# Optimization experiments

Hardware: AMD Instinct MI355X
Metric: run time of the kernel (lower is better)

## Reference

```python
import jax, jax.numpy as jnp
import numpy as np

EPS = 1e-7
FEAT_DIM = 128
N_DATA = 100000
NCE_K = 16384
NCE_T = 0.07


def _l2norm(x):
    # Normalize(power=2): x / (sum(x^2, axis=1)^(1/2))
    return x / jnp.sqrt(jnp.sum(x * x, axis=1, keepdims=True))


def _embed(x, W, b):
    return _l2norm(x @ W.T + b)


def _contrast_loss(x, n_data):
    # x: [B, K+1] of (unnormalized) probabilities; col 0 = positive
    bsz = x.shape[0]
    m = x.shape[1] - 1
    Pn = 1.0 / float(n_data)
    c = m * Pn + EPS
    log_D1 = jnp.log(x[:, 0] / (x[:, 0] + c))          # positives
    log_D0 = jnp.log((m * Pn) / (x[:, 1:] + c))         # negatives
    return -(log_D1.sum() + log_D0.sum()) / bsz


def setup_inputs() -> dict:
    key = jax.random.key(0)
    ks = jax.random.split(key, 10)
    s_dim, t_dim = 1024, 2048
    B = 64
    stdv = 1.0 / np.sqrt(FEAT_DIM / 3.0)
    inp = {
        "f_s": jax.random.normal(ks[0], (B, s_dim), dtype=jnp.float32),
        "f_t": jax.random.normal(ks[1], (B, t_dim), dtype=jnp.float32),
        "idx": jax.random.randint(ks[2], (B,), 0, N_DATA),
        "contrast_idx": jax.random.randint(ks[3], (B, NCE_K + 1), 0, N_DATA),
        # Embed params (linear): Linear(dim_in, feat_dim)
        "Ws": jax.random.normal(ks[4], (FEAT_DIM, s_dim), dtype=jnp.float32) / np.sqrt(s_dim),
        "bs": jnp.zeros((FEAT_DIM,), dtype=jnp.float32),
        "Wt": jax.random.normal(ks[5], (FEAT_DIM, t_dim), dtype=jnp.float32) / np.sqrt(t_dim),
        "bt": jnp.zeros((FEAT_DIM,), dtype=jnp.float32),
        # memory banks, init uniform(-stdv, stdv) as in CRD ContrastMemory
        "memory_v1": jax.random.uniform(ks[6], (N_DATA, FEAT_DIM), jnp.float32, -stdv, stdv),
        "memory_v2": jax.random.uniform(ks[7], (N_DATA, FEAT_DIM), jnp.float32, -stdv, stdv),
    }
    return inp


def reference(f_s, f_t, idx, contrast_idx, Ws, bs, Wt, bt, memory_v1, memory_v2):
    v_s = _embed(f_s, Ws, bs)   # [B, D]
    v_t = _embed(f_t, Wt, bt)   # [B, D]

    # idx.select(1,0).copy_(y): column 0 is the positive index
    idx_all = jnp.concatenate([idx[:, None], contrast_idx[:, 1:]], axis=1)  # [B, K+1]

    # gather from memory banks + bmm similarity
    w1 = memory_v1[idx_all]   # [B, K+1, D] (v_t side bank)
    w2 = memory_v2[idx_all]   # [B, K+1, D] (v_s side bank)
    out_t = jnp.exp(jnp.einsum('bkd,bd->bk', w1, v_t) / NCE_T)  # out_v2
    out_s = jnp.exp(jnp.einsum('bkd,bd->bk', w2, v_s) / NCE_T)  # out_v1

    # Z set on first batch: Z = out.mean() * n_data (detached constant)
    Z_s = jax.lax.stop_gradient(out_s.mean()) * N_DATA
    Z_t = jax.lax.stop_gradient(out_t.mean()) * N_DATA
    out_s = out_s / Z_s
    out_t = out_t / Z_t

    s_loss = _contrast_loss(out_s, N_DATA)
    t_loss = _contrast_loss(out_t, N_DATA)
    return s_loss + t_loss
```

## Files before the change

### kernel.cpp

```cpp
#include <hip/hip_runtime.h>

#define NDATA 100000
#define KP1 16385
#define BSZ 64
#define PTOT (BSZ * KP1)
#define NCHUNKS 6250
#define INV_T (1.0f / 0.07f)
#define ACC_STRIDE 64
#define ACC_GROUPS 32
#define SG_NWAVES 1024
#define SG_NITER 7

typedef short short8 __attribute__((ext_vector_type(8)));
typedef float f32x4 __attribute__((ext_vector_type(4)));

__device__ __forceinline__ float wave_reduce64(float v) {
    #pragma unroll
    for (int off = 32; off >= 1; off >>= 1) v += __shfl_xor(v, off);
    return v;
}

__device__ __forceinline__ float group_reduce16(float v) {
    v += __shfl_xor(v, 8); v += __shfl_xor(v, 4);
    v += __shfl_xor(v, 2); v += __shfl_xor(v, 1);
    return v;
}

__device__ __forceinline__ unsigned short f2bf(float f) {
    unsigned u = __float_as_uint(f);
    u += 0x7FFFu + ((u >> 16) & 1u);
    return (unsigned short)(u >> 16);
}

__device__ __forceinline__ float bfm(float x) {
    return __uint_as_float(((unsigned)f2bf(x)) << 16);
}

__device__ __forceinline__ short8 pack_bf16(float4 lo, float4 hi) {
    short8 r;
    r[0] = (short)f2bf(lo.x); r[1] = (short)f2bf(lo.y);
    r[2] = (short)f2bf(lo.z); r[3] = (short)f2bf(lo.w);
    r[4] = (short)f2bf(hi.x); r[5] = (short)f2bf(hi.y);
    r[6] = (short)f2bf(hi.z); r[7] = (short)f2bf(hi.w);
    return r;
}

__device__ __forceinline__ float dot4(float4 a, float4 b, float acc) {
    acc = fmaf(a.x, b.x, acc);
    acc = fmaf(a.y, b.y, acc);
    acc = fmaf(a.z, b.z, acc);
    return fmaf(a.w, b.w, acc);
}

__device__ __forceinline__ float dot8bf(const float4* a, const float4* v, int li, float d) {
    #pragma unroll
    for (int h = 0; h < 2; ++h) {
        const float4 x = a[li * 2 + h], y = v[li * 2 + h];
        d = fmaf(bfm(x.x), bfm(y.x), d);
        d = fmaf(bfm(x.y), bfm(y.y), d);
        d = fmaf(bfm(x.z), bfm(y.z), d);
        d = fmaf(bfm(x.w), bfm(y.w), d);
    }
    return d;
}

__global__ __launch_bounds__(256) void embed_kernel(
    const float* __restrict__ fs, const float* __restrict__ ft,
    const float* __restrict__ Ws, const float* __restrict__ bs,
    const float* __restrict__ Wt, const float* __restrict__ bt,
    float* __restrict__ vraw_s, float* __restrict__ vraw_t)
{
    __shared__ __align__(16) float4 FS[512];
    __shared__ __align__(16) float4 FT[1024];

    const int t  = threadIdx.x;
    const int b0 = blockIdx.y * 2;

    for (int q = t; q < 512; q += 256) {
        const int b = q >> 8, i = q & 255;
        FS[q] = ((const float4*)(fs + (size_t)(b0 + b) * 1024))[i];
    }
    for (int q = t; q < 1024; q += 256) {
        const int b = q >> 9, i = q & 511;
        FT[q] = ((const float4*)(ft + (size_t)(b0 + b) * 2048))[i];
    }
    __syncthreads();

    const int w = t >> 6, lane = t & 63;
    const int d = blockIdx.x * 4 + w;

    {
        const float4* wrow = (const float4*)(Ws + (size_t)d * 1024);
        float a0 = 0.0f, a1 = 0.0f;
        #pragma unroll
        for (int i = 0; i < 4; ++i) {
            const float4 wv = wrow[i * 64 + lane];
            a0 = dot4(wv, FS[i * 64 + lane], a0);
            a1 = dot4(wv, FS[256 + i * 64 + lane], a1);
        }
        a0 = wave_reduce64(a0) + bs[d];
        a1 = wave_reduce64(a1) + bs[d];
        if (lane == 0) {
            vraw_s[(size_t)b0 * 128 + d]       = a0;
            vraw_s[(size_t)(b0 + 1) * 128 + d] = a1;
        }
    }
    {
        const float4* wrow = (const float4*)(Wt + (size_t)d * 2048);
        float a0 = 0.0f, a1 = 0.0f;
        #pragma unroll
        for (int i = 0; i < 8; ++i) {
            const float4 wv = wrow[i * 64 + lane];
            a0 = dot4(wv, FT[i * 64 + lane], a0);
            a1 = dot4(wv, FT[512 + i * 64 + lane], a1);
        }
        a0 = wave_reduce64(a0) + bt[d];
        a1 = wave_reduce64(a1) + bt[d];
        if (lane == 0) {
            vraw_t[(size_t)b0 * 128 + d]       = a0;
            vraw_t[(size_t)(b0 + 1) * 128 + d] = a1;
        }
    }
}

__global__ __launch_bounds__(256) void norm_kernel(
    const float* __restrict__ vraw_t, const float* __restrict__ vraw_s,
    float* __restrict__ sct, float* __restrict__ scs)
{
    const float* __restrict__ v = blockIdx.x ? vraw_s : vraw_t;
    float* __restrict__ sc      = blockIdx.x ? scs : sct;
    const int t = threadIdx.x, b = t >> 2, g = t & 3;
    const float4* row = (const float4*)(v + (size_t)b * 128 + g * 32);
    float s = 0.0f;
    #pragma unroll
    for (int j = 0; j < 8; ++j) s = dot4(row[j], row[j], s);
    s += __shfl_xor(s, 1);
    s += __shfl_xor(s, 2);
    if (g == 0) sc[b] = INV_T * rsqrtf(s);
}

__global__ __launch_bounds__(256) void hist_kernel(
    const int* __restrict__ cidx, unsigned* __restrict__ cnt)
{
    const int b = blockIdx.x, part = blockIdx.y, t = threadIdx.x;
    const unsigned inc = 1u << ((b & 3) * 8);
    const int w = b >> 2;
    const int kbase = part * 1024 + 1;
    #pragma unroll
    for (int j = 0; j < 4; ++j) {
        const int row = cidx[(size_t)b * KP1 + kbase + j * 256 + t];
        atomicAdd(&cnt[(size_t)row * 16 + w], inc);
    }
}

#define SG_ISSUE(AB, CB, VM, CID)                                            \
  {                                                                          \
    const int cc_ = ((CID) < NCHUNKS) ? (CID) : (NCHUNKS - 1);               \
    VM = ((CID) < NCHUNKS) ? ~0u : 0u;                                       \
    const int r0_ = cc_ << 4;                                                \
    const float4* ar_ = (const float4*)(bankp + (size_t)(r0_ + m) * 128);    \
    _Pragma("unroll")                                                        \
    for (int kk = 0; kk < 4; ++kk) {                                         \
      AB[kk * 2]     = ar_[(kk * 4 + q4) * 2];                               \
      AB[kk * 2 + 1] = ar_[(kk * 4 + q4) * 2 + 1];                           \
    }                                                                        \
    _Pragma("unroll")                                                        \
    for (int n = 0; n < 4; ++n)                                              \
      CB[n] = cnt[(size_t)(r0_ + m) * 16 + n * 4 + q4];                      \
  }

#define SG_PROCESS(AB, CB, VM)                                               \
  {                                                                          \
    short8 af_[4];                                                           \
    _Pragma("unroll")                                                        \
    for (int kk = 0; kk < 4; ++kk)                                           \
      af_[kk] = pack_bf16(AB[kk * 2], AB[kk * 2 + 1]);                       \
    _Pragma("unroll")                                                        \
    for (int n = 0; n < 4; ++n) {                                            \
      f32x4 av = {0.f, 0.f, 0.f, 0.f};                                       \
      _Pragma("unroll")                                                      \
      for (int kk = 0; kk < 4; ++kk)                                         \
        av = __builtin_amdgcn_mfma_f32_16x16x32_bf16(bfv[n][kk], af_[kk], av, 0, 0, 0); \
      const unsigned cw_ = CB[n] & VM;                                       \
      _Pragma("unroll")                                                      \
      for (int j = 0; j < 4; ++j) {                                          \
        const float fm_ = (float)((cw_ >> (8 * j)) & 255u);                  \
        const float e_  = __expf(av[j] * scv[n][j]);                         \
        se  = fmaf(e_, fm_, se);                                             \
        se2 = fmaf(e_ * fm_, e_, se2);                                       \
      }                                                                      \
    }                                                                        \
  }

__global__ __launch_bounds__(256) void sgemm_kernel(
    const float* __restrict__ m1, const float* __restrict__ m2,
    const float* __restrict__ vraw_s, const float* __restrict__ vraw_t,
    const float* __restrict__ sct, const float* __restrict__ scs,
    const unsigned* __restrict__ cnt,
    float* __restrict__ acc)
{
    const int t = threadIdx.x;
    const int bank = blockIdx.y;
    const float* __restrict__ bankp = bank ? m2 : m1;
    const float* __restrict__ vp    = bank ? vraw_s : vraw_t;
    const float* __restrict__ scp   = bank ? scs : sct;

    const int lane = t & 63;
    const int m  = lane & 15;
    const int q4 = lane >> 4;

    short8 bfv[4][4];
    #pragma unroll
    for (int n = 0; n < 4; ++n) {
        const float4* vrow = (const float4*)(vp + (size_t)(n * 16 + m) * 128);
        #pragma unroll
        for (int kk = 0; kk < 4; ++kk) {
            const float4 lo = vrow[(kk * 4 + q4) * 2];
            const float4 hi = vrow[(kk * 4 + q4) * 2 + 1];
            bfv[n][kk] = pack_bf16(lo, hi);
        }
    }

    f32x4 scv[4];
    #pragma unroll
    for (int n = 0; n < 4; ++n) scv[n] = ((const f32x4*)scp)[n * 4 + q4];

    float se = 0.0f, se2 = 0.0f;

    const int wave = (blockIdx.x << 2) | (t >> 6);

    float4 aA[8], aB[8];
    unsigned cA[4], cB[4], vmA, vmB;

    SG_ISSUE(aA, cA, vmA, wave);
    #pragma unroll
    for (int p = 0; p < (SG_NITER - 1) / 2; ++p) {
        SG_ISSUE(aB, cB, vmB, wave + (2 * p + 1) * SG_NWAVES);
        SG_PROCESS(aA, cA, vmA);
        SG_ISSUE(aA, cA, vmA, wave + (2 * p + 2) * SG_NWAVES);
        SG_PROCESS(aB, cB, vmB);
    }
    SG_PROCESS(aA, cA, vmA);

    se  = wave_reduce64(se);
    se2 = wave_reduce64(se2);
    __shared__ float red[4][2];
    if (lane == 0) { red[t >> 6][0] = se; red[t >> 6][1] = se2; }
    __syncthreads();
    if (t < 2) {
        const float s = red[0][t] + red[1][t] + red[2][t] + red[3][t];
        atomicAdd(&acc[(blockIdx.x & (ACC_GROUPS - 1)) * ACC_STRIDE + bank * 2 + t], s);
    }
}

__global__ __launch_bounds__(256) void final_kernel(
    const int* __restrict__ idx,
    const float* __restrict__ m1, const float* __restrict__ m2,
    const float* __restrict__ vraw_t, const float* __restrict__ vraw_s,
    const float* __restrict__ sct, const float* __restrict__ scs,
    const float* __restrict__ acc, float* __restrict__ out)
{
    const int t = threadIdx.x, wave = t >> 6, lane = t & 63, g = lane >> 4, li = lane & 15;
    __shared__ float e1s[64], e2s[64];

    #pragma unroll
    for (int i = 0; i < 4; ++i) {
        const int b = wave * 16 + i * 4 + g;
        const int row = idx[b];
        float dT = dot8bf((const float4*)(m1 + (size_t)row * 128),
                          (const float4*)(vraw_t + (size_t)b * 128), li, 0.f);
        float dS = dot8bf((const float4*)(m2 + (size_t)row * 128),
                          (const float4*)(vraw_s + (size_t)b * 128), li, 0.f);
        dT = group_reduce16(dT);
        dS = group_reduce16(dS);
        if (li == 0) {
            e1s[b] = __expf(dT * sct[b]);
            e2s[b] = __expf(dS * scs[b]);
        }
    }
    __syncthreads();

    if (t < 64) {
        const int b = t;
        const float c = 0.16384f + 1e-7f;
        const float e1p = e1s[b], e2p = e2s[b];

        const float pseT = wave_reduce64(e1p);
        const float pseS = wave_reduce64(e2p);

        float seT_neg = 0.f, se2T_neg = 0.f, seS_neg = 0.f, se2S_neg = 0.f;
        for (int s = 0; s < ACC_GROUPS; ++s) {
            seT_neg  += acc[s * ACC_STRIDE + 0];
            se2T_neg += acc[s * ACC_STRIDE + 1];
            seS_neg  += acc[s * ACC_STRIDE + 2];
            se2S_neg += acc[s * ACC_STRIDE + 3];
        }

        const float zn = (float)PTOT / (float)NDATA;
        const float invZt = zn / (seT_neg + pseT);
        const float invZs = zn / (seS_neg + pseS);

        const float PB = (float)(PTOT - BSZ);
        const float LOG_MPN_C = -6.1035156e-7f;
        const float ic = 1.0f / c;

        const float negT = PB * LOG_MPN_C
                         - seT_neg * invZt * ic
                         + 0.5f * se2T_neg * invZt * invZt * ic * ic;
        const float negS = PB * LOG_MPN_C
                         - seS_neg * invZs * ic
                         + 0.5f * se2S_neg * invZs * invZs * ic * ic;

        const float x0t = e1p * invZt, x0s = e2p * invZs;
        float pos = __logf(x0t / (x0t + c)) + __logf(x0s / (x0s + c));
        pos = wave_reduce64(pos);

        if (b == 0) out[0] = -(negT + negS + pos) * (1.0f / 64.0f);
    }
}

extern "C" void kernel_launch(void* const* d_in, const int* in_sizes, int n_in,
                              void* d_out, int out_size, void* d_ws, size_t ws_size,
                              hipStream_t stream) {
    const float* fs   = (const float*)d_in[0];
    const float* ft   = (const float*)d_in[1];
    const int*   idx  = (const int*)d_in[2];
    const int*   cidx = (const int*)d_in[3];
    const float* Ws   = (const float*)d_in[4];
    const float* bs   = (const float*)d_in[5];
    const float* Wt   = (const float*)d_in[6];
    const float* bt   = (const float*)d_in[7];
    const float* m1   = (const float*)d_in[8];
    const float* m2   = (const float*)d_in[9];
    float* out = (float*)d_out;

    float* ws     = (float*)d_ws;
    float* sct    = ws;
    float* scs    = ws + 64;
    float* acc    = ws + 128;
    unsigned* cnt = (unsigned*)(ws + 4096);
    float* vraw_s = ws + 1604096;
    float* vraw_t = ws + 1612288;

    hipMemsetAsync(ws + 128, 0, (size_t)(1604096 - 128) * sizeof(float), stream);

    embed_kernel<<<dim3(32, 32), dim3(256), 0, stream>>>(
        fs, ft, Ws, bs, Wt, bt, vraw_s, vraw_t);
    norm_kernel<<<dim3(2), dim3(256), 0, stream>>>(
        vraw_t, vraw_s, sct, scs);
    hist_kernel<<<dim3(64, 16), dim3(256), 0, stream>>>(
        cidx, cnt);
    sgemm_kernel<<<dim3(256, 2), dim3(256), 0, stream>>>(
        m1, m2, vraw_s, vraw_t, sct, scs, cnt, acc);
    final_kernel<<<dim3(1), dim3(256), 0, stream>>>(
        idx, m1, m2, vraw_t, vraw_s, sct, scs, acc, out);
}
```

Baseline: 212.3 us.

## Build count histogram in shared memory and drop the large workspace memset

Replaces the global-atomic count histogram and the memset with a kernel that builds per-segment histograms in LDS (12500 bins per block) and writes them out fully, so no zeroing of the 6 MB workspace is needed. The norm computation is merged into the same launch. The count layout changes to word-major for coalesced reads, and the sgemm grid doubles to 512x2 with a shortened explicit pipeline. A bandwidth probe kernel that streams part of memory_v1 and also zeroes the accumulator is added to the timed path, which adds extra memory traffic.

```diff
diff --git a/kernel.cpp b/kernel.cpp
--- a/kernel.cpp
+++ b/kernel.cpp
@@ -8,8 +8,8 @@
 #define INV_T (1.0f / 0.07f)
 #define ACC_STRIDE 64
 #define ACC_GROUPS 32
-#define SG_NWAVES 1024
-#define SG_NITER 7
+#define SG_NW 2048
+#define HSEG 12500
 
 typedef short short8 __attribute__((ext_vector_type(8)));
 typedef float f32x4 __attribute__((ext_vector_type(4)));
@@ -62,6 +62,29 @@
         d = fmaf(bfm(x.w), bfm(y.w), d);
     }
     return d;
+}
+
+__global__ __launch_bounds__(256) void bwprobe_kernel(
+    const float* __restrict__ src, float* __restrict__ dst,
+    float* __restrict__ acc)
+{
+    const int t = threadIdx.x;
+    if (blockIdx.x < 8) {
+        acc[blockIdx.x * 256 + t] = 0.0f;
+    }
+    const int gid = blockIdx.x * 256 + t;
+    const float4* p = (const float4*)src;
+    float s = 0.0f;
+    #pragma unroll
+    for (int i = 0; i < 32; ++i) {
+        const float4 v = p[(size_t)i * 65536 + gid];
+        s += (v.x + v.y) + (v.z + v.w);
+    }
+    s = wave_reduce64(s);
+    __shared__ float r[4];
+    if ((t & 63) == 0) r[t >> 6] = s;
+    __syncthreads();
+    if (t == 0) dst[blockIdx.x] = r[0] + r[1] + r[2] + r[3];
 }
 
 __global__ __launch_bounds__(256) void embed_kernel(
@@ -123,41 +146,52 @@
     }
 }
 
-__global__ __launch_bounds__(256) void norm_kernel(
+__global__ __launch_bounds__(256) void histnorm_kernel(
+    const int* __restrict__ cidx, unsigned* __restrict__ cntw,
     const float* __restrict__ vraw_t, const float* __restrict__ vraw_s,
     float* __restrict__ sct, float* __restrict__ scs)
 {
-    const float* __restrict__ v = blockIdx.x ? vraw_s : vraw_t;
-    float* __restrict__ sc      = blockIdx.x ? scs : sct;
-    const int t = threadIdx.x, b = t >> 2, g = t & 3;
-    const float4* row = (const float4*)(v + (size_t)b * 128 + g * 32);
-    float s = 0.0f;
-    #pragma unroll
-    for (int j = 0; j < 8; ++j) s = dot4(row[j], row[j], s);
-    s += __shfl_xor(s, 1);
-    s += __shfl_xor(s, 2);
-    if (g == 0) sc[b] = INV_T * rsqrtf(s);
-}
-
-__global__ __launch_bounds__(256) void hist_kernel(
-    const int* __restrict__ cidx, unsigned* __restrict__ cnt)
-{
-    const int b = blockIdx.x, part = blockIdx.y, t = threadIdx.x;
-    const unsigned inc = 1u << ((b & 3) * 8);
-    const int w = b >> 2;
-    const int kbase = part * 1024 + 1;
-    #pragma unroll
-    for (int j = 0; j < 4; ++j) {
-        const int row = cidx[(size_t)b * KP1 + kbase + j * 256 + t];
-        atomicAdd(&cnt[(size_t)row * 16 + w], inc);
-    }
-}
-
-#define SG_ISSUE(AB, CB, VM, CID)                                            \
+    const int t = threadIdx.x;
+    if (blockIdx.x >= 128) {
+        const float* __restrict__ v = (blockIdx.x == 129) ? vraw_s : vraw_t;
+        float* __restrict__ sc      = (blockIdx.x == 129) ? scs : sct;
+        const int b = t >> 2, g = t & 3;
+        const float4* row = (const float4*)(v + (size_t)b * 128 + g * 32);
+        float s = 0.0f;
+        #pragma unroll
+        for (int j = 0; j < 8; ++j) s = dot4(row[j], row[j], s);
+        s += __shfl_xor(s, 1);
+        s += __shfl_xor(s, 2);
+        if (g == 0) sc[b] = INV_T * rsqrtf(s);
+        return;
+    }
+    const int w   = blockIdx.x >> 3;
+    const int seg = blockIdx.x & 7;
+    const int r0  = seg * HSEG;
+
+    __shared__ unsigned h[HSEG];
+    for (int i = t; i < HSEG; i += 256) h[i] = 0;
+    __syncthreads();
+
+    #pragma unroll
+    for (int j2 = 0; j2 < 4; ++j2) {
+        const int b = 4 * w + j2;
+        const unsigned inc = 1u << (8 * j2);
+        const int* __restrict__ cp = cidx + (size_t)b * KP1 + 1;
+        for (int i = t; i < 16384; i += 256) {
+            const unsigned rr = (unsigned)(cp[i] - r0);
+            if (rr < HSEG) atomicAdd(&h[rr], inc);
+        }
+    }
+    __syncthreads();
+
+    unsigned* __restrict__ dstp = cntw + (size_t)w * NDATA + r0;
+    for (int i = t; i < HSEG; i += 256) dstp[i] = h[i];
+}
+
+#define SG_ISSUE(AB, CB, CID)                                                \
   {                                                                          \
-    const int cc_ = ((CID) < NCHUNKS) ? (CID) : (NCHUNKS - 1);               \
-    VM = ((CID) < NCHUNKS) ? ~0u : 0u;                                       \
-    const int r0_ = cc_ << 4;                                                \
+    const int r0_ = (CID) << 4;                                              \
     const float4* ar_ = (const float4*)(bankp + (size_t)(r0_ + m) * 128);    \
     _Pragma("unroll")                                                        \
     for (int kk = 0; kk < 4; ++kk) {                                         \
@@ -166,10 +200,10 @@
     }                                                                        \
     _Pragma("unroll")                                                        \
     for (int n = 0; n < 4; ++n)                                              \
-      CB[n] = cnt[(size_t)(r0_ + m) * 16 + n * 4 + q4];                      \
+      CB[n] = cntw[(size_t)(n * 4 + q4) * NDATA + (r0_ + m)];                \
   }
 
-#define SG_PROCESS(AB, CB, VM)                                               \
+#define SG_PROCESS(AB, CB)                                                   \
   {                                                                          \
     short8 af_[4];                                                           \
     _Pragma("unroll")                                                        \
@@ -181,7 +215,7 @@
       _Pragma("unroll")                                                      \
       for (int kk = 0; kk < 4; ++kk)                                         \
         av = __builtin_amdgcn_mfma_f32_16x16x32_bf16(bfv[n][kk], af_[kk], av, 0, 0, 0); \
-      const unsigned cw_ = CB[n] & VM;                                       \
+      const unsigned cw_ = CB[n];                                            \
       _Pragma("unroll")                                                      \
       for (int j = 0; j < 4; ++j) {                                          \
         const float fm_ = (float)((cw_ >> (8 * j)) & 255u);                  \
@@ -196,7 +230,7 @@
     const float* __restrict__ m1, const float* __restrict__ m2,
     const float* __restrict__ vraw_s, const float* __restrict__ vraw_t,
     const float* __restrict__ sct, const float* __restrict__ scs,
-    const unsigned* __restrict__ cnt,
+    const unsigned* __restrict__ cntw,
     float* __restrict__ acc)
 {
     const int t = threadIdx.x;
@@ -230,17 +264,20 @@
     const int wave = (blockIdx.x << 2) | (t >> 6);
 
     float4 aA[8], aB[8];
-    unsigned cA[4], cB[4], vmA, vmB;
-
-    SG_ISSUE(aA, cA, vmA, wave);
-    #pragma unroll
-    for (int p = 0; p < (SG_NITER - 1) / 2; ++p) {
-        SG_ISSUE(aB, cB, vmB, wave + (2 * p + 1) * SG_NWAVES);
-        SG_PROCESS(aA, cA, vmA);
-        SG_ISSUE(aA, cA, vmA, wave + (2 * p + 2) * SG_NWAVES);
-        SG_PROCESS(aB, cB, vmB);
-    }
-    SG_PROCESS(aA, cA, vmA);
+    unsigned cA[4], cB[4];
+
+    SG_ISSUE(aA, cA, wave);
+    SG_ISSUE(aB, cB, wave + SG_NW);
+    SG_PROCESS(aA, cA);
+    SG_ISSUE(aA, cA, wave + 2 * SG_NW);
+    SG_PROCESS(aB, cB);
+    if (wave + 3 * SG_NW < NCHUNKS) {
+        SG_ISSUE(aB, cB, wave + 3 * SG_NW);
+        SG_PROCESS(aA, cA);
+        SG_PROCESS(aB, cB);
+    } else {
+        SG_PROCESS(aA, cA);
+    }
 
     se  = wave_reduce64(se);
     se2 = wave_reduce64(se2);
@@ -338,20 +375,18 @@
     float* sct    = ws;
     float* scs    = ws + 64;
     float* acc    = ws + 128;
-    unsigned* cnt = (unsigned*)(ws + 4096);
+    float* pdst   = ws + 2176;
+    unsigned* cntw = (unsigned*)(ws + 4096);
     float* vraw_s = ws + 1604096;
     float* vraw_t = ws + 1612288;
 
-    hipMemsetAsync(ws + 128, 0, (size_t)(1604096 - 128) * sizeof(float), stream);
-
+    bwprobe_kernel<<<dim3(256), dim3(256), 0, stream>>>(m1, pdst, acc);
     embed_kernel<<<dim3(32, 32), dim3(256), 0, stream>>>(
         fs, ft, Ws, bs, Wt, bt, vraw_s, vraw_t);
-    norm_kernel<<<dim3(2), dim3(256), 0, stream>>>(
-        vraw_t, vraw_s, sct, scs);
-    hist_kernel<<<dim3(64, 16), dim3(256), 0, stream>>>(
-        cidx, cnt);
-    sgemm_kernel<<<dim3(256, 2), dim3(256), 0, stream>>>(
-        m1, m2, vraw_s, vraw_t, sct, scs, cnt, acc);
+    histnorm_kernel<<<dim3(130), dim3(256), 0, stream>>>(
+        cidx, cntw, vraw_t, vraw_s, sct, scs);
+    sgemm_kernel<<<dim3(512, 2), dim3(256), 0, stream>>>(
+        m1, m2, vraw_s, vraw_t, sct, scs, cntw, acc);
     final_kernel<<<dim3(1), dim3(256), 0, stream>>>(
         idx, m1, m2, vraw_t, vraw_s, sct, scs, acc, out);
 }
```

Result: slower. 282.5 us (+33.0%).
